# Kernel optimization log

Hardware: AMD Instinct MI355X
Metric: run time of the kernel (lower is better)

Reference implementation:

```python
import jax, jax.numpy as jnp
import numpy as np

B = 524288
IN_A = 32
IN_S = 32
D = IN_A + IN_S      # combined expert input
E = 8                # num_experts
H = 64               # expert_hidden_size
GH = 32              # gating_hidden_size


def setup_inputs() -> dict:
    key = jax.random.key(0)
    ks = jax.random.split(key, 10)
    s = 0.05
    return {
        "A_data": jax.random.normal(ks[0], (B, IN_A), jnp.float32),
        "S_data": jax.random.normal(ks[1], (B, IN_S), jnp.float32),
        # gating MLP (in=IN_S -> GH -> E), weights stored as [in, out]
        "gate_w1": jax.random.normal(ks[2], (IN_S, GH), jnp.float32) * s,
        "gate_b1": jnp.zeros((GH,), jnp.float32),
        "gate_w2": jax.random.normal(ks[3], (GH, E), jnp.float32) * s,
        "gate_b2": jnp.zeros((E,), jnp.float32),
        # E expert MLPs (in=D -> H -> 1), batched over expert dim
        "exp_w1": jax.random.normal(ks[4], (E, D, H), jnp.float32) * s,
        "exp_b1": jnp.zeros((E, H), jnp.float32),
        "exp_w2": jax.random.normal(ks[5], (E, H), jnp.float32) * s,  # out=1, squeezed
        "exp_b2": jnp.zeros((E,), jnp.float32),
    }


def reference(A_data, S_data, gate_w1, gate_b1, gate_w2, gate_b2,
              exp_w1, exp_b1, exp_w2, exp_b2):
    # gating: MLP(S) -> softmax over experts
    gh = jax.nn.relu(S_data @ gate_w1 + gate_b1)                    # [B, GH]
    gating_probs = jax.nn.softmax(gh @ gate_w2 + gate_b2, axis=1)   # [B, E]
    # all experts on full batch (dense ensemble)
    x = jnp.concatenate([A_data, S_data], axis=-1)                  # [B, D]
    eh = jax.nn.relu(jnp.einsum("bd,edh->beh", x, exp_w1) + exp_b1) # [B, E, H]
    eo = jnp.einsum("beh,eh->be", eh, exp_w2) + exp_b2              # [B, E]
    # weighted sum over experts, keepdim -> [B, 1]
    return jnp.sum(eo * gating_probs, axis=1, keepdims=True)
```

## Files before the change

kernel.cpp:

```cpp
#include <hip/hip_runtime.h>
#include <hip/hip_bf16.h>
#include <math.h>

#define ROWS 256
#define DD 64
#define EE 8
#define HH 64
#define GH 32

typedef __attribute__((ext_vector_type(8))) short bf16x8;
typedef __attribute__((ext_vector_type(4))) float f32x4;

static __device__ __forceinline__ short f2bf(float f) {
    unsigned u = __builtin_bit_cast(unsigned, f);
    unsigned r = (u + 0x7fffu + ((u >> 16) & 1u)) >> 16;
    return (short)r;
}
static __device__ __forceinline__ float bf2f(unsigned short b) {
    unsigned u = ((unsigned)b) << 16;
    return __builtin_bit_cast(float, u);
}
template <int CTRL>
static __device__ __forceinline__ float dpp_add(float x) {
    int xi = __builtin_bit_cast(int, x);
    int yi = __builtin_amdgcn_update_dpp(0, xi, CTRL, 0xF, 0xF, true);
    return x + __builtin_bit_cast(float, yi);
}

__global__ __launch_bounds__(256) void prep_kernel(const float* __restrict__ ew1,
                                                   short* __restrict__ wf) {
    int idx = blockIdx.x * 256 + threadIdx.x;
    int lane = idx & 63;
    int half = (idx >> 6) & 1;
    int tt   = (idx >> 7) & 7;
    int wave = (idx >> 10) & 3;
    int n = wave * 128 + tt * 16 + (lane & 15);
    int e = n >> 6, h = n & 63;
    int quad = lane >> 4;
    short v[8];
    #pragma unroll
    for (int j = 0; j < 8; ++j) {
        int dl = quad * 8 + j + half * 32;
        v[j] = f2bf(ew1[(e * DD + dl) * HH + h]);
    }
    *(bf16x8*)(wf + (size_t)idx * 8) = *(const bf16x8*)v;
}

__global__ __launch_bounds__(256, 4) void moe_kernel(
    const float* __restrict__ A, const float* __restrict__ S,
    const float* __restrict__ gw1, const float* __restrict__ gb1,
    const float* __restrict__ gw2, const float* __restrict__ gb2,
    const short* __restrict__ wf,  const float* __restrict__ eb1,
    const float* __restrict__ ew2, const float* __restrict__ eb2,
    float* __restrict__ out)
{
    __shared__ short xs[ROWS][72];
    __shared__ unsigned short psb[ROWS][EE];

    const int t = threadIdx.x;
    const int row0 = blockIdx.x * ROWS;
    const int lane = t & 63;
    const int wave = t >> 6;
    const int quad = lane >> 4;
    const int lr = lane & 15;

    float extra;

    {
        const int row = row0 + t;
        const float* arow = A + (size_t)row * 32;
        const float* srow = S + (size_t)row * 32;
        float s[32];
        #pragma unroll
        for (int i = 0; i < 4; ++i) {
            float4 v0 = ((const float4*)arow)[2 * i];
            float4 v1 = ((const float4*)arow)[2 * i + 1];
            short v8[8] = { f2bf(v0.x), f2bf(v0.y), f2bf(v0.z), f2bf(v0.w),
                            f2bf(v1.x), f2bf(v1.y), f2bf(v1.z), f2bf(v1.w) };
            *(bf16x8*)&xs[t][i * 8] = *(const bf16x8*)v8;
        }
        #pragma unroll
        for (int i = 0; i < 4; ++i) {
            float4 v0 = ((const float4*)srow)[2 * i];
            float4 v1 = ((const float4*)srow)[2 * i + 1];
            s[i*8+0] = v0.x; s[i*8+1] = v0.y; s[i*8+2] = v0.z; s[i*8+3] = v0.w;
            s[i*8+4] = v1.x; s[i*8+5] = v1.y; s[i*8+6] = v1.z; s[i*8+7] = v1.w;
            short v8[8] = { f2bf(v0.x), f2bf(v0.y), f2bf(v0.z), f2bf(v0.w),
                            f2bf(v1.x), f2bf(v1.y), f2bf(v1.z), f2bf(v1.w) };
            *(bf16x8*)&xs[t][32 + i * 8] = *(const bf16x8*)v8;
        }
        *(float*)&xs[t][64] = 0.0f;

        float hacc[GH];
        #pragma unroll
        for (int g = 0; g < GH; ++g) hacc[g] = gb1[g];
        #pragma unroll
        for (int d = 0; d < 32; ++d) {
            float sv = s[d];
            #pragma unroll
            for (int g = 0; g < GH; ++g) hacc[g] = fmaf(sv, gw1[d * GH + g], hacc[g]);
        }
        float lg[EE];
        #pragma unroll
        for (int e = 0; e < EE; ++e) lg[e] = gb2[e];
        #pragma unroll
        for (int g = 0; g < GH; ++g) {
            float hv = fmaxf(hacc[g], 0.0f);
            #pragma unroll
            for (int e = 0; e < EE; ++e) lg[e] = fmaf(hv, gw2[g * EE + e], lg[e]);
        }
        float mx = lg[0];
        #pragma unroll
        for (int e = 1; e < EE; ++e) mx = fmaxf(mx, lg[e]);
        float sum = 0.f, pv[EE];
        #pragma unroll
        for (int e = 0; e < EE; ++e) { pv[e] = expf(lg[e] - mx); sum += pv[e]; }
        float inv = 1.0f / sum;
        unsigned short pb[EE];
        extra = 0.f;
        #pragma unroll
        for (int e = 0; e < EE; ++e) {
            float p = pv[e] * inv;
            extra = fmaf(p, eb2[e], extra);
            pb[e] = (unsigned short)f2bf(p);
        }
        *(bf16x8*)&psb[t][0] = *(const bf16x8*)pb;
    }

    bf16x8 blo[8], bhi[8];
    float w2p[8], b1c[8];
    const int e0 = wave * 2;
    #pragma unroll
    for (int tt = 0; tt < 8; ++tt) {
        const short* base = wf + ((size_t)((wave * 8 + tt) * 128) + lane) * 8;
        blo[tt] = *(const bf16x8*)base;
        bhi[tt] = *(const bf16x8*)(base + 512);
        int n = wave * 128 + tt * 16 + lr;
        int e = n >> 6, h = n & 63;
        w2p[tt] = ew2[e * HH + h];
        b1c[tt] = eb1[e * HH + h];
    }

    __syncthreads();

    #pragma unroll 1
    for (int rt = 0; rt < ROWS / 16; ++rt) {
        const short* xp = &xs[rt * 16 + lr][quad * 8];
        bf16x8 alo = *(const bf16x8*)xp;
        bf16x8 ahi = *(const bf16x8*)(xp + 32);
        f32x4 acc[8];
        #pragma unroll
        for (int tt = 0; tt < 8; ++tt) acc[tt] = (f32x4){0.f, 0.f, 0.f, 0.f};
        #pragma unroll
        for (int tt = 0; tt < 8; ++tt)
            acc[tt] = __builtin_amdgcn_mfma_f32_16x16x32_bf16(alo, blo[tt], acc[tt], 0, 0, 0);
        #pragma unroll
        for (int tt = 0; tt < 8; ++tt)
            acc[tt] = __builtin_amdgcn_mfma_f32_16x16x32_bf16(ahi, bhi[tt], acc[tt], 0, 0, 0);

        float pe0[4] = {0, 0, 0, 0}, pe1[4] = {0, 0, 0, 0};
        #pragma unroll
        for (int tt = 0; tt < 8; ++tt) {
            #pragma unroll
            for (int r = 0; r < 4; ++r) {
                float v = fmaxf(acc[tt][r] + b1c[tt], 0.0f);
                if (tt < 4) pe0[r] = fmaf(v, w2p[tt], pe0[r]);
                else        pe1[r] = fmaf(v, w2p[tt], pe1[r]);
            }
        }
        #pragma unroll
        for (int r = 0; r < 4; ++r) {
            int rw = rt * 16 + quad * 4 + r;
            float c = pe0[r] * bf2f(psb[rw][e0]) + pe1[r] * bf2f(psb[rw][e0 + 1]);
            c = dpp_add<0xB1>(c);
            c = dpp_add<0x4E>(c);
            c = dpp_add<0x124>(c);
            c = dpp_add<0x128>(c);
            if (lr == 0) atomicAdd((float*)&xs[rw][64], c);
        }
    }

    __syncthreads();
    out[row0 + t] = *(const float*)&xs[t][64] + extra;
}

extern "C" void kernel_launch(void* const* d_in, const int* in_sizes, int n_in,
                              void* d_out, int out_size, void* d_ws, size_t ws_size,
                              hipStream_t stream) {
    const float* A   = (const float*)d_in[0];
    const float* S   = (const float*)d_in[1];
    const float* gw1 = (const float*)d_in[2];
    const float* gb1 = (const float*)d_in[3];
    const float* gw2 = (const float*)d_in[4];
    const float* gb2 = (const float*)d_in[5];
    const float* ew1 = (const float*)d_in[6];
    const float* eb1 = (const float*)d_in[7];
    const float* ew2 = (const float*)d_in[8];
    const float* eb2 = (const float*)d_in[9];
    float* out = (float*)d_out;
    short* wf = (short*)d_ws;

    const int B = in_sizes[0] / 32;
    hipLaunchKernelGGL(prep_kernel, dim3(16), dim3(256), 0, stream, ew1, wf);
    hipLaunchKernelGGL(moe_kernel, dim3(B / ROWS), dim3(256), 0, stream,
                       A, S, gw1, gb1, gw2, gb2, wf, eb1, ew2, eb2, out);
}
```

Measured before the change: 194.2 us.

## Move gating MLP onto MFMA and replace LDS atomics with per-wave slots

The per-thread scalar gating MLP (32x32 FMA loop plus a 32x8 loop) is replaced with a bf16 MFMA for the first layer, using gate weights pre-packed in the prep kernel. The second layer is split across quads, reduced with ds_bpermute, and the softmax probabilities are stored to LDS in fp32. Expert bias b1 is folded into the accumulator init and b2 into the partial sums. The LDS atomicAdd is replaced by per-wave output slots that are summed at the end, and launch bounds drop to 3 blocks per CU. Gating now rounds its inputs to bf16, which slightly lowers precision, and the extra shared memory and register pressure may reduce occupancy.

```diff
diff --git a/kernel.cpp b/kernel.cpp
--- a/kernel.cpp
+++ b/kernel.cpp
@@ -6,7 +6,7 @@
 #define DD 64
 #define EE 8
 #define HH 64
-#define GH 32
+#define GHD 32
 
 typedef __attribute__((ext_vector_type(8))) short bf16x8;
 typedef __attribute__((ext_vector_type(4))) float f32x4;
@@ -16,9 +16,11 @@
     unsigned r = (u + 0x7fffu + ((u >> 16) & 1u)) >> 16;
     return (short)r;
 }
-static __device__ __forceinline__ float bf2f(unsigned short b) {
-    unsigned u = ((unsigned)b) << 16;
-    return __builtin_bit_cast(float, u);
+static __device__ __forceinline__ unsigned pk2(float lo, float hi) {
+    __hip_bfloat162 h = __float22bfloat162_rn(make_float2(lo, hi));
+    unsigned r;
+    __builtin_memcpy(&r, &h, 4);
+    return r;
 }
 template <int CTRL>
 static __device__ __forceinline__ float dpp_add(float x) {
@@ -26,8 +28,14 @@
     int yi = __builtin_amdgcn_update_dpp(0, xi, CTRL, 0xF, 0xF, true);
     return x + __builtin_bit_cast(float, yi);
 }
+static __device__ __forceinline__ float bperm_add(float x, int addr) {
+    int xi = __builtin_bit_cast(int, x);
+    int yi = __builtin_amdgcn_ds_bpermute(addr, xi);
+    return x + __builtin_bit_cast(float, yi);
+}
 
 __global__ __launch_bounds__(256) void prep_kernel(const float* __restrict__ ew1,
+                                                   const float* __restrict__ gw1,
                                                    short* __restrict__ wf) {
     int idx = blockIdx.x * 256 + threadIdx.x;
     int lane = idx & 63;
@@ -44,18 +52,27 @@
         v[j] = f2bf(ew1[(e * DD + dl) * HH + h]);
     }
     *(bf16x8*)(wf + (size_t)idx * 8) = *(const bf16x8*)v;
-}
-
-__global__ __launch_bounds__(256, 4) void moe_kernel(
+    if (idx < 128) {
+        int tile = idx >> 6;
+        int lr = lane & 15;
+        short g[8];
+        #pragma unroll
+        for (int j = 0; j < 8; ++j)
+            g[j] = f2bf(gw1[(quad * 8 + j) * GHD + tile * 16 + lr]);
+        *(bf16x8*)(wf + 32768 + (size_t)idx * 8) = *(const bf16x8*)g;
+    }
+}
+
+__global__ __launch_bounds__(256, 3) void moe_kernel(
     const float* __restrict__ A, const float* __restrict__ S,
-    const float* __restrict__ gw1, const float* __restrict__ gb1,
-    const float* __restrict__ gw2, const float* __restrict__ gb2,
-    const short* __restrict__ wf,  const float* __restrict__ eb1,
-    const float* __restrict__ ew2, const float* __restrict__ eb2,
-    float* __restrict__ out)
+    const float* __restrict__ gb1, const float* __restrict__ gw2,
+    const float* __restrict__ gb2, const short* __restrict__ wf,
+    const float* __restrict__ eb1, const float* __restrict__ ew2,
+    const float* __restrict__ eb2, float* __restrict__ out)
 {
-    __shared__ short xs[ROWS][72];
-    __shared__ unsigned short psb[ROWS][EE];
+    __shared__ __align__(16) short xs[ROWS][72];
+    __shared__ __align__(16) float ps[ROWS][EE];
+    __shared__ __align__(16) float ghs[4][16][36];
 
     const int t = threadIdx.x;
     const int row0 = blockIdx.x * ROWS;
@@ -64,67 +81,98 @@
     const int quad = lane >> 4;
     const int lr = lane & 15;
 
-    float extra;
-
     {
         const int row = row0 + t;
-        const float* arow = A + (size_t)row * 32;
-        const float* srow = S + (size_t)row * 32;
-        float s[32];
+        const float4* ar = (const float4*)(A + (size_t)row * 32);
+        const float4* sr = (const float4*)(S + (size_t)row * 32);
         #pragma unroll
         for (int i = 0; i < 4; ++i) {
-            float4 v0 = ((const float4*)arow)[2 * i];
-            float4 v1 = ((const float4*)arow)[2 * i + 1];
-            short v8[8] = { f2bf(v0.x), f2bf(v0.y), f2bf(v0.z), f2bf(v0.w),
-                            f2bf(v1.x), f2bf(v1.y), f2bf(v1.z), f2bf(v1.w) };
-            *(bf16x8*)&xs[t][i * 8] = *(const bf16x8*)v8;
+            float4 v0 = ar[2 * i], v1 = ar[2 * i + 1];
+            uint4 u;
+            u.x = pk2(v0.x, v0.y); u.y = pk2(v0.z, v0.w);
+            u.z = pk2(v1.x, v1.y); u.w = pk2(v1.z, v1.w);
+            *(uint4*)&xs[t][i * 8] = u;
         }
         #pragma unroll
         for (int i = 0; i < 4; ++i) {
-            float4 v0 = ((const float4*)srow)[2 * i];
-            float4 v1 = ((const float4*)srow)[2 * i + 1];
-            s[i*8+0] = v0.x; s[i*8+1] = v0.y; s[i*8+2] = v0.z; s[i*8+3] = v0.w;
-            s[i*8+4] = v1.x; s[i*8+5] = v1.y; s[i*8+6] = v1.z; s[i*8+7] = v1.w;
-            short v8[8] = { f2bf(v0.x), f2bf(v0.y), f2bf(v0.z), f2bf(v0.w),
-                            f2bf(v1.x), f2bf(v1.y), f2bf(v1.z), f2bf(v1.w) };
-            *(bf16x8*)&xs[t][32 + i * 8] = *(const bf16x8*)v8;
-        }
-        *(float*)&xs[t][64] = 0.0f;
-
-        float hacc[GH];
-        #pragma unroll
-        for (int g = 0; g < GH; ++g) hacc[g] = gb1[g];
-        #pragma unroll
-        for (int d = 0; d < 32; ++d) {
-            float sv = s[d];
-            #pragma unroll
-            for (int g = 0; g < GH; ++g) hacc[g] = fmaf(sv, gw1[d * GH + g], hacc[g]);
-        }
-        float lg[EE];
-        #pragma unroll
-        for (int e = 0; e < EE; ++e) lg[e] = gb2[e];
-        #pragma unroll
-        for (int g = 0; g < GH; ++g) {
-            float hv = fmaxf(hacc[g], 0.0f);
-            #pragma unroll
-            for (int e = 0; e < EE; ++e) lg[e] = fmaf(hv, gw2[g * EE + e], lg[e]);
-        }
-        float mx = lg[0];
-        #pragma unroll
-        for (int e = 1; e < EE; ++e) mx = fmaxf(mx, lg[e]);
-        float sum = 0.f, pv[EE];
-        #pragma unroll
-        for (int e = 0; e < EE; ++e) { pv[e] = expf(lg[e] - mx); sum += pv[e]; }
-        float inv = 1.0f / sum;
-        unsigned short pb[EE];
-        extra = 0.f;
-        #pragma unroll
-        for (int e = 0; e < EE; ++e) {
-            float p = pv[e] * inv;
-            extra = fmaf(p, eb2[e], extra);
-            pb[e] = (unsigned short)f2bf(p);
-        }
-        *(bf16x8*)&psb[t][0] = *(const bf16x8*)pb;
+            float4 v0 = sr[2 * i], v1 = sr[2 * i + 1];
+            uint4 u;
+            u.x = pk2(v0.x, v0.y); u.y = pk2(v0.z, v0.w);
+            u.z = pk2(v1.x, v1.y); u.w = pk2(v1.z, v1.w);
+            *(uint4*)&xs[t][32 + i * 8] = u;
+        }
+    }
+    asm volatile("s_waitcnt lgkmcnt(0)" ::: "memory");
+    __builtin_amdgcn_sched_barrier(0);
+
+    {
+        const short* gwf = wf + 32768;
+        bf16x8 gf0 = *(const bf16x8*)(gwf + (size_t)lane * 8);
+        bf16x8 gf1 = *(const bf16x8*)(gwf + 512 + (size_t)lane * 8);
+        float gw2r[8][8];
+        #pragma unroll
+        for (int j = 0; j < 8; ++j) {
+            float4 a0 = *(const float4*)(gw2 + (quad * 8 + j) * 8);
+            float4 a1 = *(const float4*)(gw2 + (quad * 8 + j) * 8 + 4);
+            gw2r[j][0] = a0.x; gw2r[j][1] = a0.y; gw2r[j][2] = a0.z; gw2r[j][3] = a0.w;
+            gw2r[j][4] = a1.x; gw2r[j][5] = a1.y; gw2r[j][6] = a1.z; gw2r[j][7] = a1.w;
+        }
+        const float gb1v0 = gb1[lr], gb1v1 = gb1[lr + 16];
+        float gb2v[8];
+        #pragma unroll
+        for (int e = 0; e < 8; ++e) gb2v[e] = gb2[e];
+        const int a16 = (lane ^ 16) << 2;
+        const int a32 = (lane ^ 32) << 2;
+
+        #pragma unroll 1
+        for (int i = 0; i < 4; ++i) {
+            const int rt = wave * 4 + i;
+            bf16x8 sa = *(const bf16x8*)&xs[rt * 16 + lr][32 + quad * 8];
+            f32x4 acc0 = {gb1v0, gb1v0, gb1v0, gb1v0};
+            f32x4 acc1 = {gb1v1, gb1v1, gb1v1, gb1v1};
+            acc0 = __builtin_amdgcn_mfma_f32_16x16x32_bf16(sa, gf0, acc0, 0, 0, 0);
+            acc1 = __builtin_amdgcn_mfma_f32_16x16x32_bf16(sa, gf1, acc1, 0, 0, 0);
+            #pragma unroll
+            for (int r = 0; r < 4; ++r) {
+                ghs[wave][quad * 4 + r][lr]      = fmaxf(acc0[r], 0.f);
+                ghs[wave][quad * 4 + r][lr + 16] = fmaxf(acc1[r], 0.f);
+            }
+            asm volatile("s_waitcnt lgkmcnt(0)" ::: "memory");
+            __builtin_amdgcn_sched_barrier(0);
+            f32x4 g0 = *(const f32x4*)&ghs[wave][lr][quad * 8];
+            f32x4 g1 = *(const f32x4*)&ghs[wave][lr][quad * 8 + 4];
+            float lg[8];
+            #pragma unroll
+            for (int e = 0; e < 8; ++e) lg[e] = 0.f;
+            #pragma unroll
+            for (int j = 0; j < 4; ++j) {
+                #pragma unroll
+                for (int e = 0; e < 8; ++e) lg[e] = fmaf(g0[j], gw2r[j][e], lg[e]);
+            }
+            #pragma unroll
+            for (int j = 0; j < 4; ++j) {
+                #pragma unroll
+                for (int e = 0; e < 8; ++e) lg[e] = fmaf(g1[j], gw2r[4 + j][e], lg[e]);
+            }
+            #pragma unroll
+            for (int e = 0; e < 8; ++e) {
+                float v = bperm_add(lg[e], a16);
+                v = bperm_add(v, a32);
+                lg[e] = v + gb2v[e];
+            }
+            float mx = fmaxf(fmaxf(fmaxf(lg[0], lg[1]), fmaxf(lg[2], lg[3])),
+                             fmaxf(fmaxf(lg[4], lg[5]), fmaxf(lg[6], lg[7])));
+            float pv[8], sum = 0.f;
+            #pragma unroll
+            for (int e = 0; e < 8; ++e) { pv[e] = __expf(lg[e] - mx); sum += pv[e]; }
+            const float inv = __builtin_amdgcn_rcpf(sum);
+            if (quad == 0) {
+                float4 p0 = make_float4(pv[0] * inv, pv[1] * inv, pv[2] * inv, pv[3] * inv);
+                float4 p1 = make_float4(pv[4] * inv, pv[5] * inv, pv[6] * inv, pv[7] * inv);
+                *(float4*)&ps[rt * 16 + lr][0] = p0;
+                *(float4*)&ps[rt * 16 + lr][4] = p1;
+            }
+        }
     }
 
     bf16x8 blo[8], bhi[8];
@@ -140,6 +188,8 @@
         w2p[tt] = ew2[e * HH + h];
         b1c[tt] = eb1[e * HH + h];
     }
+    const float ebi0 = eb2[e0] * 0.0625f;
+    const float ebi1 = eb2[e0 + 1] * 0.0625f;
 
     __syncthreads();
 
@@ -150,7 +200,8 @@
         bf16x8 ahi = *(const bf16x8*)(xp + 32);
         f32x4 acc[8];
         #pragma unroll
-        for (int tt = 0; tt < 8; ++tt) acc[tt] = (f32x4){0.f, 0.f, 0.f, 0.f};
+        for (int tt = 0; tt < 8; ++tt)
+            acc[tt] = (f32x4){b1c[tt], b1c[tt], b1c[tt], b1c[tt]};
         #pragma unroll
         for (int tt = 0; tt < 8; ++tt)
             acc[tt] = __builtin_amdgcn_mfma_f32_16x16x32_bf16(alo, blo[tt], acc[tt], 0, 0, 0);
@@ -158,30 +209,32 @@
         for (int tt = 0; tt < 8; ++tt)
             acc[tt] = __builtin_amdgcn_mfma_f32_16x16x32_bf16(ahi, bhi[tt], acc[tt], 0, 0, 0);
 
-        float pe0[4] = {0, 0, 0, 0}, pe1[4] = {0, 0, 0, 0};
+        float pe0[4] = {ebi0, ebi0, ebi0, ebi0};
+        float pe1[4] = {ebi1, ebi1, ebi1, ebi1};
         #pragma unroll
         for (int tt = 0; tt < 8; ++tt) {
             #pragma unroll
             for (int r = 0; r < 4; ++r) {
-                float v = fmaxf(acc[tt][r] + b1c[tt], 0.0f);
+                float v = fmaxf(acc[tt][r], 0.0f);
                 if (tt < 4) pe0[r] = fmaf(v, w2p[tt], pe0[r]);
                 else        pe1[r] = fmaf(v, w2p[tt], pe1[r]);
             }
         }
         #pragma unroll
         for (int r = 0; r < 4; ++r) {
-            int rw = rt * 16 + quad * 4 + r;
-            float c = pe0[r] * bf2f(psb[rw][e0]) + pe1[r] * bf2f(psb[rw][e0 + 1]);
+            const int rw = rt * 16 + quad * 4 + r;
+            float c = fmaf(pe0[r], ps[rw][e0], pe1[r] * ps[rw][e0 + 1]);
             c = dpp_add<0xB1>(c);
             c = dpp_add<0x4E>(c);
             c = dpp_add<0x124>(c);
             c = dpp_add<0x128>(c);
-            if (lr == 0) atomicAdd((float*)&xs[rw][64], c);
+            if (lr == 0) *(float*)&xs[rw][64 + 2 * wave] = c;
         }
     }
 
     __syncthreads();
-    out[row0 + t] = *(const float*)&xs[t][64] + extra;
+    const float4 fs = *(const float4*)&xs[t][64];
+    out[row0 + t] = (fs.x + fs.y) + (fs.z + fs.w);
 }
 
 extern "C" void kernel_launch(void* const* d_in, const int* in_sizes, int n_in,
@@ -201,7 +254,7 @@
     short* wf = (short*)d_ws;
 
     const int B = in_sizes[0] / 32;
-    hipLaunchKernelGGL(prep_kernel, dim3(16), dim3(256), 0, stream, ew1, wf);
+    hipLaunchKernelGGL(prep_kernel, dim3(16), dim3(256), 0, stream, ew1, gw1, wf);
     hipLaunchKernelGGL(moe_kernel, dim3(B / ROWS), dim3(256), 0, stream,
-                       A, S, gw1, gb1, gw2, gb2, wf, eb1, ew2, eb2, out);
-}
+                       A, S, gb1, gw2, gb2, wf, eb1, ew2, eb2, out);
+}
```

Measured after the change: 205.8 us. 6.0% more time.
